# Optimization experiments

Measured on AMD Instinct MI355X. Metric: run time of the kernel, lower is better.

Reference implementation:

```python
import jax, jax.numpy as jnp
import numpy as np

EMBED_DIM = 2048
NUM_HEADS = 16
HEAD_DIM = EMBED_DIM // NUM_HEADS
PROJECT_DIM = 8192


def setup_inputs() -> dict:
    key = jax.random.key(0)
    ks = jax.random.split(key, 16)
    s = 1.0 / np.sqrt(EMBED_DIM)
    sp = 1.0 / np.sqrt(PROJECT_DIM)
    return {
        "x": jax.random.normal(ks[0], (2, 2048, EMBED_DIM), jnp.float32),
        "ln1_w": jnp.ones((EMBED_DIM,), jnp.float32),
        "ln1_b": jnp.zeros((EMBED_DIM,), jnp.float32),
        "ln2_w": jnp.ones((EMBED_DIM,), jnp.float32),
        "ln2_b": jnp.zeros((EMBED_DIM,), jnp.float32),
        "wq": jax.random.normal(ks[1], (EMBED_DIM, EMBED_DIM), jnp.float32) * s,
        "bq": jnp.zeros((EMBED_DIM,), jnp.float32),
        "wk": jax.random.normal(ks[2], (EMBED_DIM, EMBED_DIM), jnp.float32) * s,
        "bk": jnp.zeros((EMBED_DIM,), jnp.float32),
        "wv": jax.random.normal(ks[3], (EMBED_DIM, EMBED_DIM), jnp.float32) * s,
        "bv": jnp.zeros((EMBED_DIM,), jnp.float32),
        "wo": jax.random.normal(ks[4], (EMBED_DIM, EMBED_DIM), jnp.float32) * s,
        "bo": jnp.zeros((EMBED_DIM,), jnp.float32),
        "w1": jax.random.normal(ks[5], (EMBED_DIM, PROJECT_DIM), jnp.float32) * s,
        "b1": jnp.zeros((PROJECT_DIM,), jnp.float32),
        "w2": jax.random.normal(ks[6], (PROJECT_DIM, EMBED_DIM), jnp.float32) * sp,
        "b2": jnpp if False else jnp.zeros((EMBED_DIM,), jnp.float32),
    }


def _layer_norm(x, w, b, eps=1e-5):
    mu = jnp.mean(x, axis=-1, keepdims=True)
    var = jnp.mean((x - mu) ** 2, axis=-1, keepdims=True)
    return (x - mu) * jax.lax.rsqrt(var + eps) * w + b


def _mha(x, wq, bq, wk, bk, wv, bv, wo, bo):
    b, s, _ = x.shape
    def split_heads(t):
        return t.reshape(b, s, NUM_HEADS, HEAD_DIM).transpose(0, 2, 1, 3)
    Q = split_heads(x @ wq + bq)
    K = split_heads(x @ wk + bk)
    V = split_heads(x @ wv + bv)
    scores = jnp.einsum('bhqd,bhkd->bhqk', Q, K) / np.sqrt(HEAD_DIM)
    causal = jnp.arange(s)[:, None] < jnp.arange(s)[None, :]  # mask future
    scores = jnp.where(causal, -jnp.inf, scores)
    att = jax.nn.softmax(scores, axis=-1)
    out = jnp.einsum('bhqk,bhkd->bhqd', att, V)
    out = out.transpose(0, 2, 1, 3).reshape(b, s, EMBED_DIM)
    return out @ wo + bo


def reference(x, ln1_w, ln1_b, ln2_w, ln2_b, wq, bq, wk, bk, wv, bv, wo, bo, w1, b1, w2, b2):
    # pre-norm, sequential: x + mlp(norm2(x + mha(norm1(x))))
    h = x + _mha(_layer_norm(x, ln1_w, ln1_b), wq, bq, wk, bk, wv, bv, wo, bo)
    m = _layer_norm(h, ln2_w, ln2_b)
    mlp = jax.nn.gelu(m @ w1 + b1) @ w2 + b2
    return h + mlp
```

## Files before the change

### kernel.cpp

```cpp
#include <hip/hip_runtime.h>

#define E_DIM 2048
#define SEQ 2048
#define BATCH 2
#define NH 16
#define HD 128
#define PD 8192
#define M_ROWS 4096
#define QKV_N 6144
#define NQT 32

typedef __attribute__((ext_vector_type(8))) short bf16x8;
typedef __attribute__((ext_vector_type(4))) float f32x4;

__device__ __forceinline__ unsigned short f2bf(float f) {
  unsigned u = __float_as_uint(f);
  u += 0x7fffu + ((u >> 16) & 1u);
  return (unsigned short)(u >> 16);
}

__device__ __forceinline__ float gelu_f(float x) {
  const float c = 0.7978845608028654f;
  return 0.5f * x * (1.0f + tanhf(c * (x + 0.044715f * x * x * x)));
}

#define GLD16(gsrc, ldst) __builtin_amdgcn_global_load_lds( \
    (const __attribute__((address_space(1))) void*)(gsrc),  \
    (__attribute__((address_space(3))) void*)(ldst), 16, 0, 0)

__global__ __launch_bounds__(256) void ln_kernel(const float* __restrict__ x,
                                                 const float* __restrict__ w,
                                                 const float* __restrict__ b,
                                                 unsigned short* __restrict__ out) {
  const int row = blockIdx.x;
  const int tid = threadIdx.x;
  const float* xr = x + (size_t)row * E_DIM;
  float4 v0 = *(const float4*)(xr + tid * 8);
  float4 v1 = *(const float4*)(xr + tid * 8 + 4);
  float s = v0.x + v0.y + v0.z + v0.w + v1.x + v1.y + v1.z + v1.w;
  float q = v0.x * v0.x + v0.y * v0.y + v0.z * v0.z + v0.w * v0.w +
            v1.x * v1.x + v1.y * v1.y + v1.z * v1.z + v1.w * v1.w;
#pragma unroll
  for (int o = 32; o; o >>= 1) { s += __shfl_xor(s, o); q += __shfl_xor(q, o); }
  __shared__ float ls[8];
  const int lane = tid & 63, wv = tid >> 6;
  if (lane == 0) { ls[wv] = s; ls[4 + wv] = q; }
  __syncthreads();
  s = ls[0] + ls[1] + ls[2] + ls[3];
  q = ls[4] + ls[5] + ls[6] + ls[7];
  const float mu = s * (1.0f / E_DIM);
  const float var = q * (1.0f / E_DIM) - mu * mu;
  const float rstd = rsqrtf(var + 1e-5f);
  float4 w0 = *(const float4*)(w + tid * 8);
  float4 w1 = *(const float4*)(w + tid * 8 + 4);
  float4 b0 = *(const float4*)(b + tid * 8);
  float4 b1 = *(const float4*)(b + tid * 8 + 4);
  ushort4 o0, o1;
  o0.x = f2bf((v0.x - mu) * rstd * w0.x + b0.x);
  o0.y = f2bf((v0.y - mu) * rstd * w0.y + b0.y);
  o0.z = f2bf((v0.z - mu) * rstd * w0.z + b0.z);
  o0.w = f2bf((v0.w - mu) * rstd * w0.w + b0.w);
  o1.x = f2bf((v1.x - mu) * rstd * w1.x + b1.x);
  o1.y = f2bf((v1.y - mu) * rstd * w1.y + b1.y);
  o1.z = f2bf((v1.z - mu) * rstd * w1.z + b1.z);
  o1.w = f2bf((v1.w - mu) * rstd * w1.w + b1.w);
  *(ushort4*)(out + (size_t)row * E_DIM + tid * 8) = o0;
  *(ushort4*)(out + (size_t)row * E_DIM + tid * 8 + 4) = o1;
}

__global__ __launch_bounds__(256) void tconv_kernel(const float* __restrict__ in,
                                                    unsigned short* __restrict__ out,
                                                    int K, int N) {
  __shared__ float t[64][65];
  const int bn = blockIdx.x, bk = blockIdx.y;
  const int tid = threadIdx.x;
  const int c4 = (tid & 15) * 4;
  const int r0 = tid >> 4;
#pragma unroll
  for (int p = 0; p < 4; ++p) {
    const int r = p * 16 + r0;
    const float4 v = *(const float4*)(in + (size_t)(bk * 64 + r) * N + bn * 64 + c4);
    t[r][c4] = v.x; t[r][c4 + 1] = v.y; t[r][c4 + 2] = v.z; t[r][c4 + 3] = v.w;
  }
  __syncthreads();
#pragma unroll
  for (int p = 0; p < 4; ++p) {
    const int rn = p * 16 + r0;
    ushort4 o;
    o.x = f2bf(t[c4][rn]);     o.y = f2bf(t[c4 + 1][rn]);
    o.z = f2bf(t[c4 + 2][rn]); o.w = f2bf(t[c4 + 3][rn]);
    *(ushort4*)(out + (size_t)(bn * 64 + rn) * K + bk * 64 + c4) = o;
  }
}

__global__ void concat3_kernel(const float* __restrict__ a, const float* __restrict__ b,
                               const float* __restrict__ c, float* __restrict__ o) {
  int i = blockIdx.x * 256 + threadIdx.x;
  if (i < E_DIM) { o[i] = a[i]; o[E_DIM + i] = b[i]; o[2 * E_DIM + i] = c[i]; }
}

template <int ACT, int RES, int OUTBF>
__global__ __launch_bounds__(256) void gemm_kernel(
    const unsigned short* __restrict__ A, const unsigned short* __restrict__ Bt,
    const float* __restrict__ bias, const float* __restrict__ res,
    void* __restrict__ Cout, int M, int N, int K) {
  __shared__ unsigned short lsA[128 * 32];
  __shared__ unsigned short lsB[128 * 32];
  const int tid = threadIdx.x;
  const int lane = tid & 63;
  const int w = tid >> 6;
  const int wr = w >> 1, wc = w & 1;
  const int bc = blockIdx.x, br = blockIdx.y;
  f32x4 acc[4][4] = {};
  const int nk = K >> 5;
  const int srow = lane >> 2;
  const int sch = lane & 3;
  const unsigned short* Abase = A + ((size_t)br * 128) * K + sch * 8;
  const unsigned short* Bbase = Bt + ((size_t)bc * 128) * K + sch * 8;

  for (int kt = 0; kt < nk; ++kt) {
    __syncthreads();
    const int kof = kt * 32;
#pragma unroll
    for (int i = 0; i < 2; ++i) {
      const int rowA = (i * 4 + w) * 16 + srow;
      GLD16(Abase + (size_t)rowA * K + kof, (char*)lsA + (i * 4 + w) * 1024);
      GLD16(Bbase + (size_t)rowA * K + kof, (char*)lsB + (i * 4 + w) * 1024);
    }
    __syncthreads();
    bf16x8 af[4], bfr[4];
#pragma unroll
    for (int mi = 0; mi < 4; ++mi) {
      const int rl = wr * 64 + mi * 16 + (lane & 15);
      af[mi] = *(const bf16x8*)(lsA + rl * 32 + (lane >> 4) * 8);
    }
#pragma unroll
    for (int ni = 0; ni < 4; ++ni) {
      const int rl = wc * 64 + ni * 16 + (lane & 15);
      bfr[ni] = *(const bf16x8*)(lsB + rl * 32 + (lane >> 4) * 8);
    }
#pragma unroll
    for (int mi = 0; mi < 4; ++mi)
#pragma unroll
      for (int ni = 0; ni < 4; ++ni)
        acc[mi][ni] = __builtin_amdgcn_mfma_f32_16x16x32_bf16(af[mi], bfr[ni], acc[mi][ni], 0, 0, 0);
  }

#pragma unroll
  for (int ni = 0; ni < 4; ++ni) {
    const int col = bc * 128 + wc * 64 + ni * 16 + (lane & 15);
    const float bv = bias[col];
#pragma unroll
    for (int mi = 0; mi < 4; ++mi) {
      const int row0 = br * 128 + wr * 64 + mi * 16 + (lane >> 4) * 4;
#pragma unroll
      for (int r = 0; r < 4; ++r) {
        const size_t idx = (size_t)(row0 + r) * N + col;
        float v = acc[mi][ni][r] + bv;
        if (RES) v += res[idx];
        if (ACT) v = gelu_f(v);
        if (OUTBF) ((unsigned short*)Cout)[idx] = f2bf(v);
        else       ((float*)Cout)[idx] = v;
      }
    }
  }
}

__global__ __launch_bounds__(256) void attn_kernel(const unsigned short* __restrict__ qkv,
                                                   unsigned short* __restrict__ out) {
  __shared__ unsigned short lsK[2][64 * 128];
  __shared__ unsigned short lsV[128 * 64];
  __shared__ unsigned short lsP[4 * 1024];
  const int tid = threadIdx.x, lane = tid & 63, w = tid >> 6;
  const int pair = blockIdx.x, bh = blockIdx.y;
  const int b = bh >> 4, h = bh & 15;
  const size_t base = (size_t)b * SEQ * QKV_N + h * HD;
  const float scale = 0.08838834764831845f;
  char* lsPw = (char*)(lsP + w * 1024);
  const int vdc = tid & 15, vkr = tid >> 4;

  for (int half = 0; half < 2; ++half) {
    const int qt = half ? (NQT - 1 - pair) : pair;
    const int q0 = qt * 64;
    const int nt = qt + 1;

    bf16x8 qf[4];
    {
      const unsigned short* qp =
          qkv + base + (size_t)(q0 + w * 16 + (lane & 15)) * QKV_N + (lane >> 4) * 8;
#pragma unroll
      for (int kk = 0; kk < 4; ++kk) qf[kk] = *(const bf16x8*)(qp + kk * 32);
    }
    f32x4 o_acc[8] = {};
    float m_r[4] = {-INFINITY, -INFINITY, -INFINITY, -INFINITY};
    float l_r[4] = {0.f, 0.f, 0.f, 0.f};
    bf16x8 vv0, vv1, vv2, vv3;

    {
#pragma unroll
      for (int i = 0; i < 4; ++i) {
        const int row = (i * 4 + w) * 4 + (lane >> 4);
        const int cs = (lane & 15) ^ (row & 7);
        GLD16(qkv + base + E_DIM + (size_t)row * QKV_N + cs * 8,
              (char*)lsK[0] + (i * 4 + w) * 1024);
      }
      const unsigned short* gv = qkv + base + 2 * E_DIM + (size_t)(vkr * 4) * QKV_N + vdc * 8;
      vv0 = *(const bf16x8*)(gv);
      vv1 = *(const bf16x8*)(gv + QKV_N);
      vv2 = *(const bf16x8*)(gv + 2 * QKV_N);
      vv3 = *(const bf16x8*)(gv + 3 * QKV_N);
    }
    __syncthreads();
#pragma unroll
    for (int e = 0; e < 8; ++e) {
      const int d = vdc * 8 + e;
      const int swz = (d & 7) ^ ((d >> 3) & 7);
      {
        const int k = vkr * 4;
        const int off = d * 128 + (((k >> 3) ^ swz) << 4) + (k & 7) * 2;
        ushort2 t2; t2.x = (unsigned short)vv0[e]; t2.y = (unsigned short)vv1[e];
        *(ushort2*)((char*)lsV + off) = t2;
      }
      {
        const int k = vkr * 4 + 2;
        const int off = d * 128 + (((k >> 3) ^ swz) << 4) + (k & 7) * 2;
        ushort2 t2; t2.x = (unsigned short)vv2[e]; t2.y = (unsigned short)vv3[e];
        *(ushort2*)((char*)lsV + off) = t2;
      }
    }

    for (int kt = 0; kt < nt; ++kt) {
      const int cur = kt & 1;
      const bool pf = (kt + 1 < nt);
      if (pf) {
        const int k0n = (kt + 1) * 64;
#pragma unroll
        for (int i = 0; i < 4; ++i) {
          const int row = (i * 4 + w) * 4 + (lane >> 4);
          const int cs = (lane & 15) ^ (row & 7);
          GLD16(qkv + base + E_DIM + (size_t)(k0n + row) * QKV_N + cs * 8,
                (char*)lsK[cur ^ 1] + (i * 4 + w) * 1024);
        }
        const unsigned short* gv =
            qkv + base + 2 * E_DIM + (size_t)(k0n + vkr * 4) * QKV_N + vdc * 8;
        vv0 = *(const bf16x8*)(gv);
        vv1 = *(const bf16x8*)(gv + QKV_N);
        vv2 = *(const bf16x8*)(gv + 2 * QKV_N);
        vv3 = *(const bf16x8*)(gv + 3 * QKV_N);
      }
      f32x4 sacc[4] = {};
#pragma unroll
      for (int kk = 0; kk < 4; ++kk) {
#pragma unroll
        for (int n = 0; n < 4; ++n) {
          const int row = n * 16 + (lane & 15);
          const int ch = (kk * 4 + (lane >> 4)) ^ (row & 7);
          bf16x8 kf = *(const bf16x8*)((const char*)lsK[cur] + row * 256 + ch * 16);
          sacc[n] = __builtin_amdgcn_mfma_f32_16x16x32_bf16(qf[kk], kf, sacc[n], 0, 0, 0);
        }
      }
      const bool diag = (kt == nt - 1);
      float p[4][4];
#pragma unroll
      for (int r = 0; r < 4; ++r) {
        float sv[4];
#pragma unroll
        for (int n = 0; n < 4; ++n) {
          float t = sacc[n][r] * scale;
          if (diag && (n * 16 + (lane & 15)) > (w * 16 + (lane >> 4) * 4 + r)) t = -INFINITY;
          sv[n] = t;
        }
        float tm = fmaxf(fmaxf(sv[0], sv[1]), fmaxf(sv[2], sv[3]));
        tm = fmaxf(tm, __shfl_xor(tm, 1));
        tm = fmaxf(tm, __shfl_xor(tm, 2));
        tm = fmaxf(tm, __shfl_xor(tm, 4));
        tm = fmaxf(tm, __shfl_xor(tm, 8));
        const float mn = fmaxf(m_r[r], tm);
        const float corr = __expf(m_r[r] - mn);
        float ps = 0.f;
#pragma unroll
        for (int n = 0; n < 4; ++n) { p[n][r] = __expf(sv[n] - mn); ps += p[n][r]; }
        ps += __shfl_xor(ps, 1); ps += __shfl_xor(ps, 2);
        ps += __shfl_xor(ps, 4); ps += __shfl_xor(ps, 8);
        l_r[r] = l_r[r] * corr + ps;
        m_r[r] = mn;
#pragma unroll
        for (int dn = 0; dn < 8; ++dn) o_acc[dn][r] *= corr;
      }
      __syncthreads();
#pragma unroll
      for (int n = 0; n < 4; ++n)
#pragma unroll
        for (int r = 0; r < 4; ++r) {
          const int prow = (lane >> 4) * 4 + r;
          const int pcol = n * 16 + (lane & 15);
          const int off = prow * 128 + ((((pcol >> 3) ^ (prow & 7))) << 4) + (pcol & 7) * 2;
          *(unsigned short*)(lsPw + off) = f2bf(p[n][r]);
        }
      bf16x8 pa[2];
#pragma unroll
      for (int ks = 0; ks < 2; ++ks) {
        const int prow = lane & 15;
        const int ch = (ks * 4 + (lane >> 4)) ^ (prow & 7);
        pa[ks] = *(const bf16x8*)(lsPw + prow * 128 + ch * 16);
      }
#pragma unroll
      for (int dn = 0; dn < 8; ++dn)
#pragma unroll
        for (int ks = 0; ks < 2; ++ks) {
          const int d = dn * 16 + (lane & 15);
          const int ch = (ks * 4 + (lane >> 4)) ^ (d & 7) ^ ((d >> 3) & 7);
          bf16x8 vf = *(const bf16x8*)((const char*)lsV + d * 128 + ch * 16);
          o_acc[dn] = __builtin_amdgcn_mfma_f32_16x16x32_bf16(pa[ks], vf, o_acc[dn], 0, 0, 0);
        }
      __syncthreads();
      if (pf) {
#pragma unroll
        for (int e = 0; e < 8; ++e) {
          const int d = vdc * 8 + e;
          const int swz = (d & 7) ^ ((d >> 3) & 7);
          {
            const int k = vkr * 4;
            const int off = d * 128 + (((k >> 3) ^ swz) << 4) + (k & 7) * 2;
            ushort2 t2; t2.x = (unsigned short)vv0[e]; t2.y = (unsigned short)vv1[e];
            *(ushort2*)((char*)lsV + off) = t2;
          }
          {
            const int k = vkr * 4 + 2;
            const int off = d * 128 + (((k >> 3) ^ swz) << 4) + (k & 7) * 2;
            ushort2 t2; t2.x = (unsigned short)vv2[e]; t2.y = (unsigned short)vv3[e];
            *(ushort2*)((char*)lsV + off) = t2;
          }
        }
      }
    }
#pragma unroll
    for (int r = 0; r < 4; ++r) {
      const float inv = 1.0f / l_r[r];
      const int row = q0 + w * 16 + (lane >> 4) * 4 + r;
      unsigned short* op = out + ((size_t)(b * SEQ + row)) * E_DIM + h * HD + (lane & 15);
#pragma unroll
      for (int dn = 0; dn < 8; ++dn) op[dn * 16] = f2bf(o_acc[dn][r] * inv);
    }
  }
}

extern "C" void kernel_launch(void* const* d_in, const int* in_sizes, int n_in,
                              void* d_out, int out_size, void* d_ws, size_t ws_size,
                              hipStream_t stream) {
  const float* x    = (const float*)d_in[0];
  const float* ln1w = (const float*)d_in[1];
  const float* ln1b = (const float*)d_in[2];
  const float* ln2w = (const float*)d_in[3];
  const float* ln2b = (const float*)d_in[4];
  const float* wq   = (const float*)d_in[5];
  const float* bq   = (const float*)d_in[6];
  const float* wk   = (const float*)d_in[7];
  const float* bk   = (const float*)d_in[8];
  const float* wv   = (const float*)d_in[9];
  const float* bv   = (const float*)d_in[10];
  const float* wo   = (const float*)d_in[11];
  const float* bo   = (const float*)d_in[12];
  const float* w1   = (const float*)d_in[13];
  const float* b1   = (const float*)d_in[14];
  const float* w2   = (const float*)d_in[15];
  const float* b2   = (const float*)d_in[16];
  (void)in_sizes; (void)n_in; (void)out_size; (void)ws_size;

  char* ws = (char*)d_ws;
  size_t off = 0;
  auto alloc = [&](size_t bytes) {
    char* p = ws + off;
    off += (bytes + 255) & ~(size_t)255;
    return p;
  };
  unsigned short* wqkv_t = (unsigned short*)alloc((size_t)QKV_N * E_DIM * 2);
  unsigned short* wo_t   = (unsigned short*)alloc((size_t)E_DIM * E_DIM * 2);
  unsigned short* w1_t   = (unsigned short*)alloc((size_t)PD * E_DIM * 2);
  unsigned short* w2_t   = (unsigned short*)alloc((size_t)E_DIM * PD * 2);
  float*          qkvb   = (float*)alloc((size_t)QKV_N * 4);
  float*          hbuf   = (float*)alloc((size_t)M_ROWS * E_DIM * 4);
  unsigned short* xn     = (unsigned short*)alloc((size_t)M_ROWS * (E_DIM + QKV_N) * 2);
  unsigned short* qkv    = xn + (size_t)M_ROWS * E_DIM;
  unsigned short* g      = xn;
  unsigned short* attn   = (unsigned short*)alloc((size_t)M_ROWS * E_DIM * 2);
  unsigned short* hn     = attn;

  tconv_kernel<<<dim3(E_DIM / 64, E_DIM / 64), 256, 0, stream>>>(wq, wqkv_t, E_DIM, E_DIM);
  tconv_kernel<<<dim3(E_DIM / 64, E_DIM / 64), 256, 0, stream>>>(wk, wqkv_t + (size_t)E_DIM * E_DIM, E_DIM, E_DIM);
  tconv_kernel<<<dim3(E_DIM / 64, E_DIM / 64), 256, 0, stream>>>(wv, wqkv_t + (size_t)2 * E_DIM * E_DIM, E_DIM, E_DIM);
  tconv_kernel<<<dim3(E_DIM / 64, E_DIM / 64), 256, 0, stream>>>(wo, wo_t, E_DIM, E_DIM);
  tconv_kernel<<<dim3(PD / 64, E_DIM / 64), 256, 0, stream>>>(w1, w1_t, E_DIM, PD);
  tconv_kernel<<<dim3(E_DIM / 64, PD / 64), 256, 0, stream>>>(w2, w2_t, PD, E_DIM);
  concat3_kernel<<<dim3(E_DIM / 256), 256, 0, stream>>>(bq, bk, bv, qkvb);

  ln_kernel<<<dim3(M_ROWS), 256, 0, stream>>>(x, ln1w, ln1b, xn);
  gemm_kernel<0, 0, 1><<<dim3(QKV_N / 128, M_ROWS / 128), 256, 0, stream>>>(
      xn, wqkv_t, qkvb, nullptr, qkv, M_ROWS, QKV_N, E_DIM);
  attn_kernel<<<dim3(NQT / 2, BATCH * NH), 256, 0, stream>>>(qkv, attn);

  gemm_kernel<0, 1, 0><<<dim3(E_DIM / 128, M_ROWS / 128), 256, 0, stream>>>(
      attn, wo_t, bo, x, hbuf, M_ROWS, E_DIM, E_DIM);
  ln_kernel<<<dim3(M_ROWS), 256, 0, stream>>>(hbuf, ln2w, ln2b, hn);
  gemm_kernel<1, 0, 1><<<dim3(PD / 128, M_ROWS / 128), 256, 0, stream>>>(
      hn, w1_t, b1, nullptr, g, M_ROWS, PD, E_DIM);
  gemm_kernel<0, 1, 0><<<dim3(E_DIM / 128, M_ROWS / 128), 256, 0, stream>>>(
      g, w2_t, b2, hbuf, (float*)d_out, M_ROWS, E_DIM, PD);
}
```

Measured before the change: 991.4 us.

## Replace 128x128 GEMM with double-buffered 256x256 tile GEMM using swizzled LDS

After: 971.7 us. -2.0%, faster.

```diff
diff --git a/kernel.cpp b/kernel.cpp
--- a/kernel.cpp
+++ b/kernel.cpp
@@ -99,64 +99,104 @@
   if (i < E_DIM) { o[i] = a[i]; o[E_DIM + i] = b[i]; o[2 * E_DIM + i] = c[i]; }
 }
 
+#define STAGE_A(d, kt) do {                                                   \
+  const unsigned short* Ab_ = A + (size_t)(br * 256) * K + (size_t)(kt) * 64 + srcCh * 8; \
+  _Pragma("unroll") for (int j_ = 0; j_ < 4; ++j_)                            \
+    GLD16(Ab_ + (size_t)(j_ * 64 + (tid >> 3)) * K,                           \
+          smem + (d) * 65536 + j_ * 8192 + wid * 1024);                       \
+} while (0)
+
+#define STAGE_B(d, kt) do {                                                   \
+  const unsigned short* Bb_ = Bt + (size_t)(bc * 256) * K + (size_t)(kt) * 64 + srcCh * 8; \
+  _Pragma("unroll") for (int j_ = 0; j_ < 4; ++j_)                            \
+    GLD16(Bb_ + (size_t)(j_ * 64 + (tid >> 3)) * K,                           \
+          smem + (d) * 65536 + 32768 + j_ * 8192 + wid * 1024);               \
+} while (0)
+
+#define LDA_Q(d, mh) do {                                                     \
+  const char* ab_ = smem + (d) * 65536;                                       \
+  _Pragma("unroll") for (int mf_ = 0; mf_ < 4; ++mf_) {                       \
+    const int row_ = wm * 128 + (mh) * 64 + mf_ * 16 + (lane & 15);           \
+    _Pragma("unroll") for (int ks_ = 0; ks_ < 2; ++ks_) {                     \
+      const int ch_ = (ks_ * 4 + (lane >> 4)) ^ (row_ & 7);                   \
+      aq[mf_ * 2 + ks_] = *(const bf16x8*)(ab_ + row_ * 128 + ch_ * 16);      \
+    } }                                                                       \
+} while (0)
+
+#define LDB_Q(d, nh, bq) do {                                                 \
+  const char* bb_ = smem + (d) * 65536 + 32768;                               \
+  _Pragma("unroll") for (int nf_ = 0; nf_ < 2; ++nf_) {                       \
+    const int row_ = wn * 64 + (nh) * 32 + nf_ * 16 + (lane & 15);            \
+    _Pragma("unroll") for (int ks_ = 0; ks_ < 2; ++ks_) {                     \
+      const int ch_ = (ks_ * 4 + (lane >> 4)) ^ (row_ & 7);                   \
+      bq[nf_ * 2 + ks_] = *(const bf16x8*)(bb_ + row_ * 128 + ch_ * 16);      \
+    } }                                                                       \
+} while (0)
+
+#define MMQ(mh, nh, bq) do {                                                  \
+  __builtin_amdgcn_s_setprio(1);                                              \
+  _Pragma("unroll") for (int mf_ = 0; mf_ < 4; ++mf_)                         \
+  _Pragma("unroll") for (int nf_ = 0; nf_ < 2; ++nf_)                         \
+  _Pragma("unroll") for (int ks_ = 0; ks_ < 2; ++ks_)                         \
+    acc[(mh) * 4 + mf_][(nh) * 2 + nf_] = __builtin_amdgcn_mfma_f32_16x16x32_bf16( \
+        aq[mf_ * 2 + ks_], bq[nf_ * 2 + ks_], acc[(mh) * 4 + mf_][(nh) * 2 + nf_], 0, 0, 0); \
+  __builtin_amdgcn_s_setprio(0);                                              \
+} while (0)
+
 template <int ACT, int RES, int OUTBF>
-__global__ __launch_bounds__(256) void gemm_kernel(
+__global__ __launch_bounds__(512, 2) void gemm256_kernel(
     const unsigned short* __restrict__ A, const unsigned short* __restrict__ Bt,
     const float* __restrict__ bias, const float* __restrict__ res,
-    void* __restrict__ Cout, int M, int N, int K) {
-  __shared__ unsigned short lsA[128 * 32];
-  __shared__ unsigned short lsB[128 * 32];
-  const int tid = threadIdx.x;
-  const int lane = tid & 63;
-  const int w = tid >> 6;
-  const int wr = w >> 1, wc = w & 1;
-  const int bc = blockIdx.x, br = blockIdx.y;
-  f32x4 acc[4][4] = {};
-  const int nk = K >> 5;
-  const int srow = lane >> 2;
-  const int sch = lane & 3;
-  const unsigned short* Abase = A + ((size_t)br * 128) * K + sch * 8;
-  const unsigned short* Bbase = Bt + ((size_t)bc * 128) * K + sch * 8;
-
-  for (int kt = 0; kt < nk; ++kt) {
+    void* __restrict__ Cout, int M, int N, int K, int nbc) {
+  extern __shared__ char smem[];
+  const int tid = threadIdx.x, lane = tid & 63, wid = tid >> 6;
+  const int wm = wid >> 2, wn = wid & 3;
+  const int cpx = gridDim.x >> 3;
+  const int bid = (blockIdx.x & 7) * cpx + (blockIdx.x >> 3);
+  const int br = bid / nbc, bc = bid % nbc;
+  const int srcCh = (tid & 7) ^ ((tid >> 3) & 7);
+
+  f32x4 acc[8][4] = {};
+  bf16x8 aq[8], bq0[4], bq1[4];
+
+  const int NT = K >> 6;
+  STAGE_A(0, 0);
+  STAGE_B(0, 0);
+  for (int t = 0; t < NT; ++t) {
+    const int cur = t & 1;
+    const bool pf = (t + 1 < NT);
     __syncthreads();
-    const int kof = kt * 32;
-#pragma unroll
-    for (int i = 0; i < 2; ++i) {
-      const int rowA = (i * 4 + w) * 16 + srow;
-      GLD16(Abase + (size_t)rowA * K + kof, (char*)lsA + (i * 4 + w) * 1024);
-      GLD16(Bbase + (size_t)rowA * K + kof, (char*)lsB + (i * 4 + w) * 1024);
-    }
-    __syncthreads();
-    bf16x8 af[4], bfr[4];
-#pragma unroll
-    for (int mi = 0; mi < 4; ++mi) {
-      const int rl = wr * 64 + mi * 16 + (lane & 15);
-      af[mi] = *(const bf16x8*)(lsA + rl * 32 + (lane >> 4) * 8);
-    }
-#pragma unroll
-    for (int ni = 0; ni < 4; ++ni) {
-      const int rl = wc * 64 + ni * 16 + (lane & 15);
-      bfr[ni] = *(const bf16x8*)(lsB + rl * 32 + (lane >> 4) * 8);
-    }
-#pragma unroll
-    for (int mi = 0; mi < 4; ++mi)
-#pragma unroll
-      for (int ni = 0; ni < 4; ++ni)
-        acc[mi][ni] = __builtin_amdgcn_mfma_f32_16x16x32_bf16(af[mi], bfr[ni], acc[mi][ni], 0, 0, 0);
+    LDA_Q(cur, 0);
+    LDB_Q(cur, 0, bq0);
+    if (pf) STAGE_A(cur ^ 1, t + 1);
+    __builtin_amdgcn_s_barrier();
+    MMQ(0, 0, bq0);
+    __builtin_amdgcn_s_barrier();
+    LDB_Q(cur, 1, bq1);
+    if (pf) STAGE_B(cur ^ 1, t + 1);
+    __builtin_amdgcn_s_barrier();
+    MMQ(0, 1, bq1);
+    __builtin_amdgcn_s_barrier();
+    LDA_Q(cur, 1);
+    __builtin_amdgcn_s_barrier();
+    MMQ(1, 1, bq1);
+    __builtin_amdgcn_s_barrier();
+    LDB_Q(cur, 0, bq0);
+    __builtin_amdgcn_s_barrier();
+    MMQ(1, 0, bq0);
   }
 
 #pragma unroll
-  for (int ni = 0; ni < 4; ++ni) {
-    const int col = bc * 128 + wc * 64 + ni * 16 + (lane & 15);
+  for (int nfg = 0; nfg < 4; ++nfg) {
+    const int col = bc * 256 + wn * 64 + nfg * 16 + (lane & 15);
     const float bv = bias[col];
 #pragma unroll
-    for (int mi = 0; mi < 4; ++mi) {
-      const int row0 = br * 128 + wr * 64 + mi * 16 + (lane >> 4) * 4;
+    for (int mfg = 0; mfg < 8; ++mfg) {
+      const int row0 = br * 256 + wm * 128 + mfg * 16 + (lane >> 4) * 4;
 #pragma unroll
       for (int r = 0; r < 4; ++r) {
         const size_t idx = (size_t)(row0 + r) * N + col;
-        float v = acc[mi][ni][r] + bv;
+        float v = acc[mfg][nfg][r] + bv;
         if (RES) v += res[idx];
         if (ACT) v = gelu_f(v);
         if (OUTBF) ((unsigned short*)Cout)[idx] = f2bf(v);
@@ -386,6 +426,13 @@
   unsigned short* attn   = (unsigned short*)alloc((size_t)M_ROWS * E_DIM * 2);
   unsigned short* hn     = attn;
 
+  hipFuncSetAttribute((const void*)gemm256_kernel<0, 0, 1>,
+                      hipFuncAttributeMaxDynamicSharedMemorySize, 131072);
+  hipFuncSetAttribute((const void*)gemm256_kernel<0, 1, 0>,
+                      hipFuncAttributeMaxDynamicSharedMemorySize, 131072);
+  hipFuncSetAttribute((const void*)gemm256_kernel<1, 0, 1>,
+                      hipFuncAttributeMaxDynamicSharedMemorySize, 131072);
+
   tconv_kernel<<<dim3(E_DIM / 64, E_DIM / 64), 256, 0, stream>>>(wq, wqkv_t, E_DIM, E_DIM);
   tconv_kernel<<<dim3(E_DIM / 64, E_DIM / 64), 256, 0, stream>>>(wk, wqkv_t + (size_t)E_DIM * E_DIM, E_DIM, E_DIM);
   tconv_kernel<<<dim3(E_DIM / 64, E_DIM / 64), 256, 0, stream>>>(wv, wqkv_t + (size_t)2 * E_DIM * E_DIM, E_DIM, E_DIM);
@@ -395,15 +442,15 @@
   concat3_kernel<<<dim3(E_DIM / 256), 256, 0, stream>>>(bq, bk, bv, qkvb);
 
   ln_kernel<<<dim3(M_ROWS), 256, 0, stream>>>(x, ln1w, ln1b, xn);
-  gemm_kernel<0, 0, 1><<<dim3(QKV_N / 128, M_ROWS / 128), 256, 0, stream>>>(
-      xn, wqkv_t, qkvb, nullptr, qkv, M_ROWS, QKV_N, E_DIM);
+  gemm256_kernel<0, 0, 1><<<dim3((M_ROWS / 256) * (QKV_N / 256)), 512, 131072, stream>>>(
+      xn, wqkv_t, qkvb, nullptr, qkv, M_ROWS, QKV_N, E_DIM, QKV_N / 256);
   attn_kernel<<<dim3(NQT / 2, BATCH * NH), 256, 0, stream>>>(qkv, attn);
 
-  gemm_kernel<0, 1, 0><<<dim3(E_DIM / 128, M_ROWS / 128), 256, 0, stream>>>(
-      attn, wo_t, bo, x, hbuf, M_ROWS, E_DIM, E_DIM);
+  gemm256_kernel<0, 1, 0><<<dim3((M_ROWS / 256) * (E_DIM / 256)), 512, 131072, stream>>>(
+      attn, wo_t, bo, x, hbuf, M_ROWS, E_DIM, E_DIM, E_DIM / 256);
   ln_kernel<<<dim3(M_ROWS), 256, 0, stream>>>(hbuf, ln2w, ln2b, hn);
-  gemm_kernel<1, 0, 1><<<dim3(PD / 128, M_ROWS / 128), 256, 0, stream>>>(
-      hn, w1_t, b1, nullptr, g, M_ROWS, PD, E_DIM);
-  gemm_kernel<0, 1, 0><<<dim3(E_DIM / 128, M_ROWS / 128), 256, 0, stream>>>(
-      g, w2_t, b2, hbuf, (float*)d_out, M_ROWS, E_DIM, PD);
-}
+  gemm256_kernel<1, 0, 1><<<dim3((M_ROWS / 256) * (PD / 256)), 512, 131072, stream>>>(
+      hn, w1_t, b1, nullptr, g, M_ROWS, PD, E_DIM, PD / 256);
+  gemm256_kernel<0, 1, 0><<<dim3((M_ROWS / 256) * (E_DIM / 256)), 512, 131072, stream>>>(
+      g, w2_t, b2, hbuf, (float*)d_out, M_ROWS, E_DIM, PD, E_DIM / 256);
+}
```
